# Kernel optimization log

Hardware: AMD Instinct MI355X
Metric: run time of the kernel (lower is better)

## Reference

```python
import jax, jax.numpy as jnp
import numpy as np

B, S, H = 4, 2048, 1024   # batch, seq_len, hidden_dim
E, D = 8, 1024            # num_experts, expert_dim (== hidden per module structure)
TOP_K = 2


def setup_inputs() -> dict:
    key = jax.random.key(0)
    ks = jax.random.split(key, 8)
    scale_h = 1.0 / np.sqrt(H)
    scale_d = 1.0 / np.sqrt(D)
    return {
        "x": jax.random.normal(ks[0], (B, S, H), dtype=jnp.float32),
        # router linear: hidden -> num_experts
        "w_router": jax.random.normal(ks[1], (H, E), dtype=jnp.float32) * scale_h,
        "b_router": jnp.zeros((E,), dtype=jnp.float32),
        # per-expert linear: hidden -> expert_dim
        "w_experts": jax.random.normal(ks[2], (E, H, D), dtype=jnp.float32) * scale_h,
        "b_experts": jnp.zeros((E, D), dtype=jnp.float32),
        # output linear: expert_dim -> expert_dim
        "w_out": jax.random.normal(ks[3], (D, D), dtype=jnp.float32) * scale_d,
        "b_out": jnp.zeros((D,), dtype=jnp.float32),
    }


def reference(x, w_router, b_router, w_experts, b_experts, w_out, b_out):
    # --- MoERouter: softmax over expert logits, top-2, renormalize ---
    logits = jnp.einsum("bsh,he->bse", x, w_router) + b_router          # [B,S,E]
    probs = jax.nn.softmax(logits, axis=-1)
    top_p, top_i = jax.lax.top_k(probs, TOP_K)                           # [B,S,2]
    top_p = top_p / jnp.sum(top_p, axis=-1, keepdims=True)
    # --- Dense expert compute over all tokens (module computes every expert) ---
    expert_out = jnp.einsum("bsh,ehd->bsed", x, w_experts) + b_experts   # [B,S,E,D]
    expert_out = jax.nn.gelu(expert_out)
    # --- Gather top-2 expert outputs and combine with routing weights ---
    sel = jnp.take_along_axis(expert_out, top_i[..., None], axis=2)      # [B,S,2,D]
    combined = jnp.sum(sel * top_p[..., None], axis=2)                   # [B,S,D]
    # --- Output projection ---
    return jnp.einsum("bsd,de->bse", combined, w_out) + b_out
```

## Files before the change

kernel.cpp:

```cpp
#include <hip/hip_runtime.h>


#define TOKENS 8192
#define HDIM   1024
#define DDIM   1024
#define NEXP   8

typedef __bf16 bf16x8 __attribute__((ext_vector_type(8)));
typedef float  f32x4  __attribute__((ext_vector_type(4)));

__device__ __forceinline__ unsigned short f2b(float f) {
  unsigned int u = __builtin_bit_cast(unsigned int, f);
  u = u + 0x7fffu + ((u >> 16) & 1u);
  return (unsigned short)(u >> 16);
}
__device__ __forceinline__ float b2f(unsigned short b) {
  unsigned int u = ((unsigned int)b) << 16;
  return __builtin_bit_cast(float, u);
}

__device__ __forceinline__ void gld_lds16(const void* g, void* l) {
  __builtin_amdgcn_global_load_lds(
      (__attribute__((address_space(1))) void*)(g),
      (__attribute__((address_space(3))) void*)(l),
      16, 0, 0);
}


__global__ void transpose_cvt_kernel(const float* __restrict__ we, const float* __restrict__ wo,
                                     unsigned short* __restrict__ weT, unsigned short* __restrict__ woT) {
  __shared__ unsigned short tile[32][33];
  int z = blockIdx.z;
  const float* s;
  unsigned short* d;
  if (z < 8) { s = we + (size_t)z * HDIM * DDIM; d = weT + (size_t)z * HDIM * DDIM; }
  else       { s = wo;                            d = woT; }
  int bx = blockIdx.x * 32;
  int by = blockIdx.y * 32;
  for (int i = threadIdx.y; i < 32; i += 8)
    tile[i][threadIdx.x] = f2b(s[(size_t)(by + i) * 1024 + bx + threadIdx.x]);
  __syncthreads();
  for (int i = threadIdx.y; i < 32; i += 8)
    d[(size_t)(bx + i) * 1024 + by + threadIdx.x] = tile[threadIdx.x][i];
}


__global__ void router_compute_kernel(const float* __restrict__ x, const float* __restrict__ wr,
                                      const float* __restrict__ br,
                                      int* __restrict__ eidx, float* __restrict__ ew,
                                      unsigned short* __restrict__ xb) {
  int wave = threadIdx.x >> 6, lane = threadIdx.x & 63;
  int t = blockIdx.x * 4 + wave;
  const float* xp = x + (size_t)t * HDIM;
  unsigned short* xbp = xb + (size_t)t * HDIM;
  float acc[8];
#pragma unroll
  for (int e = 0; e < 8; ++e) acc[e] = 0.f;
#pragma unroll
  for (int h0 = 0; h0 < HDIM; h0 += 256) {
    int h = h0 + lane * 4;
    float4 xv = *(const float4*)&xp[h];
    ushort4 o;
    o.x = f2b(xv.x); o.y = f2b(xv.y); o.z = f2b(xv.z); o.w = f2b(xv.w);
    *(ushort4*)&xbp[h] = o;
    float xq[4] = {xv.x, xv.y, xv.z, xv.w};
#pragma unroll
    for (int q = 0; q < 4; ++q) {
      const float4* wp = (const float4*)&wr[(h + q) * 8];
      float4 w0 = wp[0], w1 = wp[1];
      acc[0] += xq[q] * w0.x; acc[1] += xq[q] * w0.y; acc[2] += xq[q] * w0.z; acc[3] += xq[q] * w0.w;
      acc[4] += xq[q] * w1.x; acc[5] += xq[q] * w1.y; acc[6] += xq[q] * w1.z; acc[7] += xq[q] * w1.w;
    }
  }
#pragma unroll
  for (int off = 32; off; off >>= 1)
#pragma unroll
    for (int e = 0; e < 8; ++e) acc[e] += __shfl_xor(acc[e], off, 64);
  if (lane == 0) {
    float l[8], p[8];
    float m = -1e30f;
#pragma unroll
    for (int e = 0; e < 8; ++e) { l[e] = acc[e] + br[e]; m = fmaxf(m, l[e]); }
    float s = 0.f;
#pragma unroll
    for (int e = 0; e < 8; ++e) { p[e] = __expf(l[e] - m); s += p[e]; }
    int i1 = 0;
#pragma unroll
    for (int e = 1; e < 8; ++e) if (p[e] > p[i1]) i1 = e;
    int i2 = (i1 == 0) ? 1 : 0;
#pragma unroll
    for (int e = 0; e < 8; ++e) if (e != i1 && p[e] > p[i2]) i2 = e;
    float ps = p[i1] + p[i2];
    eidx[t * 2]     = i1;  ew[t * 2]     = p[i1] / ps;
    eidx[t * 2 + 1] = i2;  ew[t * 2 + 1] = p[i2] / ps;
  }
}


__global__ __launch_bounds__(1024) void build_lists_kernel(
    const int* __restrict__ eidx, const float* ew,
    int* __restrict__ counts, int* __restrict__ tok2, float* __restrict__ wl,
    int* s2p) {
  int e = blockIdx.x;
  int tid = threadIdx.x;
  int lane = tid & 63, wv = tid >> 6;
  __shared__ int wsum[16];
  __shared__ int base;
  if (tid == 0) base = 0;
  __syncthreads();
  for (int c = 0; c < 2 * TOKENS; c += 1024) {
    int i = c + tid;
    bool m = (eidx[i] == e);
    unsigned long long bal = __ballot(m);
    if (lane == 0) wsum[wv] = __popcll(bal);
    __syncthreads();
    int wbase = base;
    for (int w = 0; w < wv; ++w) wbase += wsum[w];
    if (m) {
      int pos = wbase + __popcll(bal & ((1ull << lane) - 1ull));
      float w = ew[i];
      tok2[e * TOKENS + pos] = i;
      wl[e * TOKENS + pos] = w;
      s2p[i] = pos;
    }
    int total = 0;
#pragma unroll
    for (int w = 0; w < 16; ++w) total += wsum[w];
    __syncthreads();
    if (tid == 0) base += total;
    __syncthreads();
  }
  if (tid == 0) counts[e] = base;
}


__global__ __launch_bounds__(256, 3) void expert_gemm_kernel(
    const unsigned short* __restrict__ xb, const unsigned short* __restrict__ weT,
    const float* __restrict__ b_experts, const int* __restrict__ counts,
    const int* __restrict__ tok2, const float* __restrict__ wlist,
    unsigned short* __restrict__ outE) {
  int b = blockIdx.x;
  int id = (b >> 3) + (b & 7) * 512;
  int e = id >> 9;
  int rem = id & 511;
  int m0 = (rem >> 3) << 7;
  int n0 = (rem & 7) << 7;
  int cnt = counts[e];
  if (m0 >= cnt) return;
  int cbase = 0;
  for (int q = 0; q < e; ++q) cbase += counts[q];

  __shared__ unsigned short As[3][128 * 32];
  __shared__ unsigned short Bs[3][128 * 32];
  __shared__ int   tokS[128];
  __shared__ float wS[128];

  int tid = threadIdx.x;
  if (tid < 128) {
    int r = m0 + tid;
    tokS[tid] = (r < cnt) ? tok2[e * TOKENS + r] : 0;
    wS[tid]   = (r < cnt) ? wlist[e * TOKENS + r] : 0.f;
  }
  __syncthreads();

  int wave = tid >> 6, lane = tid & 63;
  int subr = lane >> 2, koff = (lane & 3) * 8;

  const unsigned short* wbase = weT + (size_t)e * (HDIM * DDIM);
  const unsigned short* asrc[2];
  const unsigned short* bsrc[2];
  unsigned short* adst[3][2];
  unsigned short* bdst[3][2];
#pragma unroll
  for (int i = 0; i < 2; ++i) {
    int row = i * 64 + wave * 16 + subr;
    asrc[i] = xb + (size_t)(tokS[row] >> 1) * HDIM + koff;
    bsrc[i] = wbase + (size_t)(n0 + row) * HDIM + koff;
#pragma unroll
    for (int bb = 0; bb < 3; ++bb) {
      adst[bb][i] = &As[bb][i * 2048 + wave * 512];
      bdst[bb][i] = &Bs[bb][i * 2048 + wave * 512];
    }
  }

  int wm = wave & 1, wn = wave >> 1;
  int quad = lane >> 4, lr = lane & 15;

  f32x4 zero = {0.f, 0.f, 0.f, 0.f};
  f32x4 acc[4][4];
#pragma unroll
  for (int i = 0; i < 4; ++i)
#pragma unroll
    for (int j = 0; j < 4; ++j) acc[i][j] = zero;

#pragma unroll
  for (int s = 0; s < 2; ++s)
#pragma unroll
    for (int i = 0; i < 2; ++i) {
      gld_lds16(asrc[i] + s * 32, adst[s][i]);
      gld_lds16(bsrc[i] + s * 32, bdst[s][i]);
    }

#pragma unroll
  for (int kk = 0; kk < 32; ++kk) {
    if (kk < 31) asm volatile("s_waitcnt vmcnt(4)" ::: "memory");
    else         asm volatile("s_waitcnt vmcnt(0)" ::: "memory");
    __builtin_amdgcn_s_barrier();
    if (kk + 2 < 32) {
      int nb = (kk + 2) % 3;
      int off = (kk + 2) * 32;
#pragma unroll
      for (int i = 0; i < 2; ++i) {
        gld_lds16(asrc[i] + off, adst[nb][i]);
        gld_lds16(bsrc[i] + off, bdst[nb][i]);
      }
    }
    int cb = kk % 3;
    bf16x8 af[4], bfr[4];
#pragma unroll
    for (int i = 0; i < 4; ++i)
      af[i] = *(const bf16x8*)&As[cb][(wm * 64 + i * 16 + lr) * 32 + quad * 8];
#pragma unroll
    for (int j = 0; j < 4; ++j)
      bfr[j] = *(const bf16x8*)&Bs[cb][(wn * 64 + j * 16 + lr) * 32 + quad * 8];
#pragma unroll
    for (int i = 0; i < 4; ++i)
#pragma unroll
      for (int j = 0; j < 4; ++j)
        acc[i][j] = __builtin_amdgcn_mfma_f32_16x16x32_bf16(af[i], bfr[j], acc[i][j], 0, 0, 0);
  }

  int rowbase = cbase + m0;
#pragma unroll
  for (int j = 0; j < 4; ++j) {
    int col = n0 + wn * 64 + j * 16 + lr;
    float bias = b_experts[e * DDIM + col];
#pragma unroll
    for (int i = 0; i < 4; ++i) {
      int rbase = wm * 64 + i * 16 + quad * 4;
#pragma unroll
      for (int r = 0; r < 4; ++r) {
        int row = rbase + r;
        if (m0 + row < cnt) {
          float h = acc[i][j][r] + bias;
          float z = 0.7978845608f * (h + 0.044715f * h * h * h);
          float t = 1.f - 2.f / (__expf(2.f * z) + 1.f);
          float g = 0.5f * h * (1.f + t);
          outE[(size_t)(rowbase + row) * DDIM + col] = f2b(g * wS[row]);
        }
      }
    }
  }
}


__global__ void combine_kernel(const ushort4* __restrict__ outE,
                               const int* __restrict__ eidx, const int* __restrict__ s2p,
                               const int* __restrict__ counts,
                               ushort4* __restrict__ comb) {
  __shared__ int cbase[8];
  int tid = threadIdx.x;
  if (tid < 8) {
    int s = 0;
    for (int q = 0; q < tid; ++q) s += counts[q];
    cbase[tid] = s;
  }
  __syncthreads();
  int t = blockIdx.x;
  int d4 = tid;
  int i0 = t * 2, i1 = i0 + 1;
  size_t r0 = ((size_t)(cbase[eidx[i0]] + s2p[i0])) * 256 + d4;
  size_t r1 = ((size_t)(cbase[eidx[i1]] + s2p[i1])) * 256 + d4;
  ushort4 a = outE[r0];
  ushort4 b = outE[r1];
  ushort4 o;
  o.x = f2b(b2f(a.x) + b2f(b.x));
  o.y = f2b(b2f(a.y) + b2f(b.y));
  o.z = f2b(b2f(a.z) + b2f(b.z));
  o.w = f2b(b2f(a.w) + b2f(b.w));
  comb[t * 256 + d4] = o;
}


__global__ __launch_bounds__(256, 3) void out_gemm_kernel(
    const unsigned short* __restrict__ Abf, const unsigned short* __restrict__ BT,
    const float* __restrict__ bias, float* __restrict__ out) {
  int b = blockIdx.x;
  int id = (b >> 3) + (b & 7) * 64;
  int n0 = (id >> 6) << 7;
  int m0 = (id & 63) << 7;

  __shared__ unsigned short As[3][128 * 32];
  __shared__ unsigned short Bs[3][128 * 32];
  int tid = threadIdx.x, wave = tid >> 6, lane = tid & 63;
  int subr = lane >> 2, koff = (lane & 3) * 8;

  const unsigned short* asrc[2];
  const unsigned short* bsrc[2];
  unsigned short* adst[3][2];
  unsigned short* bdst[3][2];
#pragma unroll
  for (int i = 0; i < 2; ++i) {
    int row = i * 64 + wave * 16 + subr;
    asrc[i] = Abf + (size_t)(m0 + row) * DDIM + koff;
    bsrc[i] = BT + (size_t)(n0 + row) * DDIM + koff;
#pragma unroll
    for (int bb = 0; bb < 3; ++bb) {
      adst[bb][i] = &As[bb][i * 2048 + wave * 512];
      bdst[bb][i] = &Bs[bb][i * 2048 + wave * 512];
    }
  }

  int wm = wave & 1, wn = wave >> 1;
  int quad = lane >> 4, lr = lane & 15;

  f32x4 zero = {0.f, 0.f, 0.f, 0.f};
  f32x4 acc[4][4];
#pragma unroll
  for (int i = 0; i < 4; ++i)
#pragma unroll
    for (int j = 0; j < 4; ++j) acc[i][j] = zero;

#pragma unroll
  for (int s = 0; s < 2; ++s)
#pragma unroll
    for (int i = 0; i < 2; ++i) {
      gld_lds16(asrc[i] + s * 32, adst[s][i]);
      gld_lds16(bsrc[i] + s * 32, bdst[s][i]);
    }

#pragma unroll
  for (int kk = 0; kk < 32; ++kk) {
    if (kk < 31) asm volatile("s_waitcnt vmcnt(4)" ::: "memory");
    else         asm volatile("s_waitcnt vmcnt(0)" ::: "memory");
    __builtin_amdgcn_s_barrier();
    if (kk + 2 < 32) {
      int nb = (kk + 2) % 3;
      int off = (kk + 2) * 32;
#pragma unroll
      for (int i = 0; i < 2; ++i) {
        gld_lds16(asrc[i] + off, adst[nb][i]);
        gld_lds16(bsrc[i] + off, bdst[nb][i]);
      }
    }
    int cb = kk % 3;
    bf16x8 af[4], bfr[4];
#pragma unroll
    for (int i = 0; i < 4; ++i)
      af[i] = *(const bf16x8*)&As[cb][(wm * 64 + i * 16 + lr) * 32 + quad * 8];
#pragma unroll
    for (int j = 0; j < 4; ++j)
      bfr[j] = *(const bf16x8*)&Bs[cb][(wn * 64 + j * 16 + lr) * 32 + quad * 8];
#pragma unroll
    for (int i = 0; i < 4; ++i)
#pragma unroll
      for (int j = 0; j < 4; ++j)
        acc[i][j] = __builtin_amdgcn_mfma_f32_16x16x32_bf16(af[i], bfr[j], acc[i][j], 0, 0, 0);
  }

#pragma unroll
  for (int j = 0; j < 4; ++j) {
    int col = n0 + wn * 64 + j * 16 + lr;
    float bs = bias[col];
#pragma unroll
    for (int i = 0; i < 4; ++i) {
      int rbase = wm * 64 + i * 16 + quad * 4;
#pragma unroll
      for (int r = 0; r < 4; ++r)
        out[(size_t)(m0 + rbase + r) * DDIM + col] = acc[i][j][r] + bs;
    }
  }
}


extern "C" void kernel_launch(void* const* d_in, const int* in_sizes, int n_in,
                              void* d_out, int out_size, void* d_ws, size_t ws_size,
                              hipStream_t stream) {
  const float* x  = (const float*)d_in[0];
  const float* wr = (const float*)d_in[1];
  const float* br = (const float*)d_in[2];
  const float* we = (const float*)d_in[3];
  const float* be = (const float*)d_in[4];
  const float* wo = (const float*)d_in[5];
  const float* bo = (const float*)d_in[6];
  float* out = (float*)d_out;

  char* ws = (char*)d_ws;
  unsigned short* xb      = (unsigned short*)(ws);
  unsigned short* weT     = (unsigned short*)(ws + 16777216);
  unsigned short* woT     = (unsigned short*)(ws + 33554432);
  unsigned short* outE    = (unsigned short*)(ws + 35651584);
  int*            counts  = (int*)           (ws + 69206016);
  int*            tok2    = (int*)           (ws + 69206272);
  float*          wlist   = (float*)         (ws + 69468416);
  int*            eidx    = (int*)           (ws + 69730560);
  float*          ew      = (float*)         (ws + 69796096);
  int*            s2p     = (int*)ew;
  unsigned short* comb    = xb;

  router_compute_kernel<<<2048, 256, 0, stream>>>(x, wr, br, eidx, ew, xb);
  transpose_cvt_kernel<<<dim3(32, 32, 9), dim3(32, 8), 0, stream>>>(we, wo, weT, woT);
  build_lists_kernel<<<8, 1024, 0, stream>>>(eidx, ew, counts, tok2, wlist, s2p);
  expert_gemm_kernel<<<4096, 256, 0, stream>>>(xb, weT, be, counts, tok2, wlist, outE);
  combine_kernel<<<8192, 256, 0, stream>>>((const ushort4*)outE, eidx, s2p, counts, (ushort4*)comb);
  out_gemm_kernel<<<512, 256, 0, stream>>>(comb, woT, bo, out);
}
```

Before: 282.3 us.

## Restructure expert GEMM into 256x256 tiles with 8 waves and phased pipeline

The grouped expert GEMM moves from 128x128 tiles with 4 waves to 256x256 tiles with 8 waves. Each wave now computes 128x64 outputs through a 4-phase schedule per 64-wide K step, interleaving global-to-LDS loads with MFMA bursts that run under raised priority. The LDS layout is XOR-swizzled to cut bank conflicts, and the block-to-expert mapping now interleaves experts. The larger tiles raise data reuse and reduce global traffic, but they also mean more padded work wasted on each expert's partial last M tile and higher register pressure.

```diff
diff --git a/kernel.cpp b/kernel.cpp
--- a/kernel.cpp
+++ b/kernel.cpp
@@ -134,119 +134,135 @@
 }
 
 
-__global__ __launch_bounds__(256, 3) void expert_gemm_kernel(
+#define MFMA_ROW(MH, MI, AF) \
+  acc[(MH)*4+(MI)][0] = __builtin_amdgcn_mfma_f32_16x16x32_bf16(AF, bF0, acc[(MH)*4+(MI)][0], 0, 0, 0); \
+  acc[(MH)*4+(MI)][1] = __builtin_amdgcn_mfma_f32_16x16x32_bf16(AF, bF1, acc[(MH)*4+(MI)][1], 0, 0, 0); \
+  acc[(MH)*4+(MI)][2] = __builtin_amdgcn_mfma_f32_16x16x32_bf16(AF, bF2, acc[(MH)*4+(MI)][2], 0, 0, 0); \
+  acc[(MH)*4+(MI)][3] = __builtin_amdgcn_mfma_f32_16x16x32_bf16(AF, bF3, acc[(MH)*4+(MI)][3], 0, 0, 0);
+
+#define PHASE(KS, MH, STAGE_CODE, TRAIL_CODE) do { \
+  const int abase_ = (cur * 2 + (KS)) * 8192; \
+  const bf16x8 aF0 = *(const bf16x8*)&As[abase_ + (arow0 + (MH)*64 +  0) * 32 + cs8]; \
+  const bf16x8 aF1 = *(const bf16x8*)&As[abase_ + (arow0 + (MH)*64 + 16) * 32 + cs8]; \
+  const bf16x8 aF2 = *(const bf16x8*)&As[abase_ + (arow0 + (MH)*64 + 32) * 32 + cs8]; \
+  const bf16x8 aF3 = *(const bf16x8*)&As[abase_ + (arow0 + (MH)*64 + 48) * 32 + cs8]; \
+  const bf16x8 bF0 = *(const bf16x8*)&Bs[abase_ + (brow0 +  0) * 32 + cs8]; \
+  const bf16x8 bF1 = *(const bf16x8*)&Bs[abase_ + (brow0 + 16) * 32 + cs8]; \
+  const bf16x8 bF2 = *(const bf16x8*)&Bs[abase_ + (brow0 + 32) * 32 + cs8]; \
+  const bf16x8 bF3 = *(const bf16x8*)&Bs[abase_ + (brow0 + 48) * 32 + cs8]; \
+  STAGE_CODE; \
+  asm volatile("" ::: "memory"); \
+  __builtin_amdgcn_s_barrier(); \
+  __builtin_amdgcn_s_setprio(1); \
+  MFMA_ROW(MH, 0, aF0) \
+  MFMA_ROW(MH, 1, aF1) \
+  MFMA_ROW(MH, 2, aF2) \
+  MFMA_ROW(MH, 3, aF3) \
+  __builtin_amdgcn_s_setprio(0); \
+  TRAIL_CODE; \
+  asm volatile("" ::: "memory"); \
+  __builtin_amdgcn_s_barrier(); \
+} while (0)
+
+__global__ __launch_bounds__(512, 2) void expert_gemm_kernel(
     const unsigned short* __restrict__ xb, const unsigned short* __restrict__ weT,
     const float* __restrict__ b_experts, const int* __restrict__ counts,
     const int* __restrict__ tok2, const float* __restrict__ wlist,
     unsigned short* __restrict__ outE) {
   int b = blockIdx.x;
-  int id = (b >> 3) + (b & 7) * 512;
-  int e = id >> 9;
-  int rem = id & 511;
-  int m0 = (rem >> 3) << 7;
-  int n0 = (rem & 7) << 7;
+  int e = b & 7;
+  int tt = b >> 3;
+  int m0 = (tt >> 2) << 8;
+  int n0 = (tt & 3) << 8;
   int cnt = counts[e];
   if (m0 >= cnt) return;
   int cbase = 0;
   for (int q = 0; q < e; ++q) cbase += counts[q];
 
-  __shared__ unsigned short As[3][128 * 32];
-  __shared__ unsigned short Bs[3][128 * 32];
-  __shared__ int   tokS[128];
-  __shared__ float wS[128];
+  __shared__ unsigned short As[2 * 2 * 8192];
+  __shared__ unsigned short Bs[2 * 2 * 8192];
+  __shared__ int   tokS[256];
+  __shared__ float wS[256];
 
   int tid = threadIdx.x;
-  if (tid < 128) {
+  if (tid < 256) {
     int r = m0 + tid;
     tokS[tid] = (r < cnt) ? tok2[e * TOKENS + r] : 0;
     wS[tid]   = (r < cnt) ? wlist[e * TOKENS + r] : 0.f;
   }
   __syncthreads();
 
-  int wave = tid >> 6, lane = tid & 63;
-  int subr = lane >> 2, koff = (lane & 3) * 8;
-
   const unsigned short* wbase = weT + (size_t)e * (HDIM * DDIM);
-  const unsigned short* asrc[2];
-  const unsigned short* bsrc[2];
-  unsigned short* adst[3][2];
-  unsigned short* bdst[3][2];
-#pragma unroll
-  for (int i = 0; i < 2; ++i) {
-    int row = i * 64 + wave * 16 + subr;
-    asrc[i] = xb + (size_t)(tokS[row] >> 1) * HDIM + koff;
-    bsrc[i] = wbase + (size_t)(n0 + row) * HDIM + koff;
-#pragma unroll
-    for (int bb = 0; bb < 3; ++bb) {
-      adst[bb][i] = &As[bb][i * 2048 + wave * 512];
-      bdst[bb][i] = &Bs[bb][i * 2048 + wave * 512];
-    }
-  }
-
-  int wm = wave & 1, wn = wave >> 1;
-  int quad = lane >> 4, lr = lane & 15;
-
-  f32x4 zero = {0.f, 0.f, 0.f, 0.f};
-  f32x4 acc[4][4];
-#pragma unroll
-  for (int i = 0; i < 4; ++i)
-#pragma unroll
-    for (int j = 0; j < 4; ++j) acc[i][j] = zero;
-
-#pragma unroll
-  for (int s = 0; s < 2; ++s)
-#pragma unroll
-    for (int i = 0; i < 2; ++i) {
-      gld_lds16(asrc[i] + s * 32, adst[s][i]);
-      gld_lds16(bsrc[i] + s * 32, bdst[s][i]);
-    }
-
-#pragma unroll
-  for (int kk = 0; kk < 32; ++kk) {
-    if (kk < 31) asm volatile("s_waitcnt vmcnt(4)" ::: "memory");
-    else         asm volatile("s_waitcnt vmcnt(0)" ::: "memory");
-    __builtin_amdgcn_s_barrier();
-    if (kk + 2 < 32) {
-      int nb = (kk + 2) % 3;
-      int off = (kk + 2) * 32;
-#pragma unroll
-      for (int i = 0; i < 2; ++i) {
-        gld_lds16(asrc[i] + off, adst[nb][i]);
-        gld_lds16(bsrc[i] + off, bdst[nb][i]);
-      }
-    }
-    int cb = kk % 3;
-    bf16x8 af[4], bfr[4];
-#pragma unroll
-    for (int i = 0; i < 4; ++i)
-      af[i] = *(const bf16x8*)&As[cb][(wm * 64 + i * 16 + lr) * 32 + quad * 8];
-#pragma unroll
-    for (int j = 0; j < 4; ++j)
-      bfr[j] = *(const bf16x8*)&Bs[cb][(wn * 64 + j * 16 + lr) * 32 + quad * 8];
-#pragma unroll
-    for (int i = 0; i < 4; ++i)
-#pragma unroll
-      for (int j = 0; j < 4; ++j)
-        acc[i][j] = __builtin_amdgcn_mfma_f32_16x16x32_bf16(af[i], bfr[j], acc[i][j], 0, 0, 0);
+  int g0 = tid, g1 = 512 + tid;
+  int r0 = g0 >> 2, r1 = g1 >> 2;
+  int sc0 = (((g0 & 3) ^ (r0 & 3)) << 3);
+  int sc1 = (((g1 & 3) ^ (r1 & 3)) << 3);
+  const unsigned short* aS0 = xb + (size_t)(tokS[r0] >> 1) * HDIM + sc0;
+  const unsigned short* aS1 = xb + (size_t)(tokS[r1] >> 1) * HDIM + sc1;
+  const unsigned short* bS0 = wbase + (size_t)(n0 + r0) * HDIM + sc0;
+  const unsigned short* bS1 = wbase + (size_t)(n0 + r1) * HDIM + sc1;
+  int du0 = (tid & ~63) * 8;
+  int du1 = (512 + (tid & ~63)) * 8;
+
+  int wid = tid >> 6, lane = tid & 63;
+  int wm = wid >> 2, wn = wid & 3;
+  int lr = lane & 15, quad = lane >> 4;
+  int cs8 = ((quad ^ (lane & 3)) << 3);
+  int arow0 = wm * 128 + lr;
+  int brow0 = wn * 64 + lr;
+
+  f32x4 acc[8][4];
+#pragma unroll
+  for (int i = 0; i < 8; ++i)
+#pragma unroll
+    for (int j = 0; j < 4; ++j) acc[i][j] = (f32x4){0.f, 0.f, 0.f, 0.f};
+
+  gld_lds16(aS0 +  0, &As[0 * 8192 + du0]); gld_lds16(aS1 +  0, &As[0 * 8192 + du1]);
+  gld_lds16(bS0 +  0, &Bs[0 * 8192 + du0]); gld_lds16(bS1 +  0, &Bs[0 * 8192 + du1]);
+  gld_lds16(aS0 + 32, &As[1 * 8192 + du0]); gld_lds16(aS1 + 32, &As[1 * 8192 + du1]);
+  gld_lds16(bS0 + 32, &Bs[1 * 8192 + du0]); gld_lds16(bS1 + 32, &Bs[1 * 8192 + du1]);
+  gld_lds16(aS0 + 64, &As[2 * 8192 + du0]); gld_lds16(aS1 + 64, &As[2 * 8192 + du1]);
+  gld_lds16(bS0 + 64, &Bs[2 * 8192 + du0]); gld_lds16(bS1 + 64, &Bs[2 * 8192 + du1]);
+  __syncthreads();
+
+  for (int t = 0; t < 16; ++t) {
+    int cur = t & 1;
+    PHASE(0, 0,
+      { if (t < 15) { int kc = (t + 1) * 64 + 32; int db = ((cur ^ 1) * 2 + 1) * 8192;
+          gld_lds16(aS0 + kc, &As[db + du0]); gld_lds16(aS1 + kc, &As[db + du1]); } },
+      { });
+    PHASE(0, 1,
+      { if (t < 15) { int kc = (t + 1) * 64 + 32; int db = ((cur ^ 1) * 2 + 1) * 8192;
+          gld_lds16(bS0 + kc, &Bs[db + du0]); gld_lds16(bS1 + kc, &Bs[db + du1]); } },
+      { if (t < 15) asm volatile("s_waitcnt vmcnt(4)" ::: "memory");
+        else        asm volatile("s_waitcnt vmcnt(0)" ::: "memory"); });
+    PHASE(1, 0,
+      { if (t < 14) { int kc = (t + 2) * 64; int db = (cur * 2) * 8192;
+          gld_lds16(aS0 + kc, &As[db + du0]); gld_lds16(aS1 + kc, &As[db + du1]); } },
+      { });
+    PHASE(1, 1,
+      { if (t < 14) { int kc = (t + 2) * 64; int db = (cur * 2) * 8192;
+          gld_lds16(bS0 + kc, &Bs[db + du0]); gld_lds16(bS1 + kc, &Bs[db + du1]); } },
+      { asm volatile("s_waitcnt vmcnt(8)" ::: "memory"); });
   }
 
   int rowbase = cbase + m0;
 #pragma unroll
-  for (int j = 0; j < 4; ++j) {
-    int col = n0 + wn * 64 + j * 16 + lr;
+  for (int ni = 0; ni < 4; ++ni) {
+    int col = n0 + wn * 64 + ni * 16 + lr;
     float bias = b_experts[e * DDIM + col];
 #pragma unroll
-    for (int i = 0; i < 4; ++i) {
-      int rbase = wm * 64 + i * 16 + quad * 4;
+    for (int am = 0; am < 8; ++am) {
+      int rb = wm * 128 + am * 16 + quad * 4;
 #pragma unroll
       for (int r = 0; r < 4; ++r) {
-        int row = rbase + r;
+        int row = rb + r;
         if (m0 + row < cnt) {
-          float h = acc[i][j][r] + bias;
+          float h = acc[am][ni][r] + bias;
           float z = 0.7978845608f * (h + 0.044715f * h * h * h);
-          float t = 1.f - 2.f / (__expf(2.f * z) + 1.f);
-          float g = 0.5f * h * (1.f + t);
-          outE[(size_t)(rowbase + row) * DDIM + col] = f2b(g * wS[row]);
+          float tz = 1.f - 2.f / (__expf(2.f * z) + 1.f);
+          float gg = 0.5f * h * (1.f + tz);
+          outE[(size_t)(rowbase + row) * DDIM + col] = f2b(gg * wS[row]);
         }
       }
     }
@@ -401,7 +417,7 @@
   router_compute_kernel<<<2048, 256, 0, stream>>>(x, wr, br, eidx, ew, xb);
   transpose_cvt_kernel<<<dim3(32, 32, 9), dim3(32, 8), 0, stream>>>(we, wo, weT, woT);
   build_lists_kernel<<<8, 1024, 0, stream>>>(eidx, ew, counts, tok2, wlist, s2p);
-  expert_gemm_kernel<<<4096, 256, 0, stream>>>(xb, weT, be, counts, tok2, wlist, outE);
+  expert_gemm_kernel<<<1024, 512, 0, stream>>>(xb, weT, be, counts, tok2, wlist, outE);
   combine_kernel<<<8192, 256, 0, stream>>>((const ushort4*)outE, eidx, s2p, counts, (ushort4*)comb);
   out_gemm_kernel<<<512, 256, 0, stream>>>(comb, woT, bo, out);
 }
```

New measurement: 330.2 us. 1.17x slower.

## Fuse router, weight transpose and list building into one pre-kernel using atomics

Applied to the files above, without the earlier changes.

Merges the router, the weight transpose/convert and the expert list construction into a single launch, with block ranges split by role. The serial 8-block list-building kernel is replaced by per-token atomicAdd slot allocation on the expert counters, which are zeroed by a memset. This removes two launches and a low-parallelism scan pass. The cost is that token order inside each expert list becomes nondeterministic, and atomics contend on eight counters.

```diff
diff --git a/kernel.cpp b/kernel.cpp
--- a/kernel.cpp
+++ b/kernel.cpp
@@ -27,29 +27,35 @@
 }
 
 
-__global__ void transpose_cvt_kernel(const float* __restrict__ we, const float* __restrict__ wo,
-                                     unsigned short* __restrict__ weT, unsigned short* __restrict__ woT) {
+__global__ __launch_bounds__(256) void pre_kernel(
+    const float* __restrict__ x, const float* __restrict__ wr,
+    const float* __restrict__ br,
+    const float* __restrict__ we, const float* __restrict__ wo,
+    unsigned short* __restrict__ weT, unsigned short* __restrict__ woT,
+    unsigned short* __restrict__ xb,
+    int* __restrict__ eidx, int* __restrict__ counts,
+    int* __restrict__ tok2, float* __restrict__ wlist, int* __restrict__ s2p) {
   __shared__ unsigned short tile[32][33];
-  int z = blockIdx.z;
-  const float* s;
-  unsigned short* d;
-  if (z < 8) { s = we + (size_t)z * HDIM * DDIM; d = weT + (size_t)z * HDIM * DDIM; }
-  else       { s = wo;                            d = woT; }
-  int bx = blockIdx.x * 32;
-  int by = blockIdx.y * 32;
-  for (int i = threadIdx.y; i < 32; i += 8)
-    tile[i][threadIdx.x] = f2b(s[(size_t)(by + i) * 1024 + bx + threadIdx.x]);
-  __syncthreads();
-  for (int i = threadIdx.y; i < 32; i += 8)
-    d[(size_t)(bx + i) * 1024 + by + threadIdx.x] = tile[threadIdx.x][i];
-}
-
-
-__global__ void router_compute_kernel(const float* __restrict__ x, const float* __restrict__ wr,
-                                      const float* __restrict__ br,
-                                      int* __restrict__ eidx, float* __restrict__ ew,
-                                      unsigned short* __restrict__ xb) {
-  int wave = threadIdx.x >> 6, lane = threadIdx.x & 63;
+  int tid = threadIdx.x;
+  if (blockIdx.x >= 2048) {
+    int lid = blockIdx.x - 2048;
+    int z = lid >> 10;
+    int rem = lid & 1023;
+    int bx = (rem & 31) * 32;
+    int by = (rem >> 5) * 32;
+    const float* s;
+    unsigned short* d;
+    if (z < 8) { s = we + (size_t)z * HDIM * DDIM; d = weT + (size_t)z * HDIM * DDIM; }
+    else       { s = wo;                            d = woT; }
+    int tx = tid & 31, ty = tid >> 5;
+    for (int i = ty; i < 32; i += 8)
+      tile[i][tx] = f2b(s[(size_t)(by + i) * 1024 + bx + tx]);
+    __syncthreads();
+    for (int i = ty; i < 32; i += 8)
+      d[(size_t)(bx + i) * 1024 + by + tx] = tile[tx][i];
+    return;
+  }
+  int wave = tid >> 6, lane = tid & 63;
   int t = blockIdx.x * 4 + wave;
   const float* xp = x + (size_t)t * HDIM;
   unsigned short* xbp = xb + (size_t)t * HDIM;
@@ -91,46 +97,13 @@
 #pragma unroll
     for (int e = 0; e < 8; ++e) if (e != i1 && p[e] > p[i2]) i2 = e;
     float ps = p[i1] + p[i2];
-    eidx[t * 2]     = i1;  ew[t * 2]     = p[i1] / ps;
-    eidx[t * 2 + 1] = i2;  ew[t * 2 + 1] = p[i2] / ps;
-  }
-}
-
-
-__global__ __launch_bounds__(1024) void build_lists_kernel(
-    const int* __restrict__ eidx, const float* ew,
-    int* __restrict__ counts, int* __restrict__ tok2, float* __restrict__ wl,
-    int* s2p) {
-  int e = blockIdx.x;
-  int tid = threadIdx.x;
-  int lane = tid & 63, wv = tid >> 6;
-  __shared__ int wsum[16];
-  __shared__ int base;
-  if (tid == 0) base = 0;
-  __syncthreads();
-  for (int c = 0; c < 2 * TOKENS; c += 1024) {
-    int i = c + tid;
-    bool m = (eidx[i] == e);
-    unsigned long long bal = __ballot(m);
-    if (lane == 0) wsum[wv] = __popcll(bal);
-    __syncthreads();
-    int wbase = base;
-    for (int w = 0; w < wv; ++w) wbase += wsum[w];
-    if (m) {
-      int pos = wbase + __popcll(bal & ((1ull << lane) - 1ull));
-      float w = ew[i];
-      tok2[e * TOKENS + pos] = i;
-      wl[e * TOKENS + pos] = w;
-      s2p[i] = pos;
-    }
-    int total = 0;
-#pragma unroll
-    for (int w = 0; w < 16; ++w) total += wsum[w];
-    __syncthreads();
-    if (tid == 0) base += total;
-    __syncthreads();
-  }
-  if (tid == 0) counts[e] = base;
+    int p1 = atomicAdd(&counts[i1], 1);
+    int p2 = atomicAdd(&counts[i2], 1);
+    eidx[t * 2]     = i1;
+    eidx[t * 2 + 1] = i2;
+    tok2[i1 * TOKENS + p1] = t * 2;      wlist[i1 * TOKENS + p1] = p[i1] / ps;  s2p[t * 2]     = p1;
+    tok2[i2 * TOKENS + p2] = t * 2 + 1;  wlist[i2 * TOKENS + p2] = p[i2] / ps;  s2p[t * 2 + 1] = p2;
+  }
 }
 
 
@@ -394,13 +367,12 @@
   int*            tok2    = (int*)           (ws + 69206272);
   float*          wlist   = (float*)         (ws + 69468416);
   int*            eidx    = (int*)           (ws + 69730560);
-  float*          ew      = (float*)         (ws + 69796096);
-  int*            s2p     = (int*)ew;
+  int*            s2p     = (int*)           (ws + 69796096);
   unsigned short* comb    = xb;
 
-  router_compute_kernel<<<2048, 256, 0, stream>>>(x, wr, br, eidx, ew, xb);
-  transpose_cvt_kernel<<<dim3(32, 32, 9), dim3(32, 8), 0, stream>>>(we, wo, weT, woT);
-  build_lists_kernel<<<8, 1024, 0, stream>>>(eidx, ew, counts, tok2, wlist, s2p);
+  hipMemsetAsync(counts, 0, NEXP * sizeof(int), stream);
+  pre_kernel<<<2048 + 9216, 256, 0, stream>>>(x, wr, br, we, wo, weT, woT,
+                                              xb, eidx, counts, tok2, wlist, s2p);
   expert_gemm_kernel<<<4096, 256, 0, stream>>>(xb, weT, be, counts, tok2, wlist, outE);
   combine_kernel<<<8192, 256, 0, stream>>>((const ushort4*)outE, eidx, s2p, counts, (ushort4*)comb);
   out_gemm_kernel<<<512, 256, 0, stream>>>(comb, woT, bo, out);
```

Result: slower. 420.3 us (+48.9%).

## Fuse top-2 combine into output GEMM A-load and merge router with weight transpose

Applied to the files above, without the earlier changes.

The separate combine kernel is removed. The output GEMM now gathers the two expert rows per token through registers, sums them in bf16 and writes the result to LDS as its A tile, using a double buffer instead of the triple-buffered async LDS loads. The router and the weight transpose/convert kernels are merged into one launch with a block-index split. This saves the combine write/read round trip and one launch, at the cost of register-path A loads, a shallower pipeline and an extra full barrier per k-step in the GEMM.

```diff
diff --git a/kernel.cpp b/kernel.cpp
--- a/kernel.cpp
+++ b/kernel.cpp
@@ -8,6 +8,7 @@
 
 typedef __bf16 bf16x8 __attribute__((ext_vector_type(8)));
 typedef float  f32x4  __attribute__((ext_vector_type(4)));
+typedef unsigned short u16x8 __attribute__((ext_vector_type(8)));
 
 __device__ __forceinline__ unsigned short f2b(float f) {
   unsigned int u = __builtin_bit_cast(unsigned int, f);
@@ -27,29 +28,34 @@
 }
 
 
-__global__ void transpose_cvt_kernel(const float* __restrict__ we, const float* __restrict__ wo,
-                                     unsigned short* __restrict__ weT, unsigned short* __restrict__ woT) {
+__global__ __launch_bounds__(256) void pre_kernel(
+    const float* __restrict__ x, const float* __restrict__ wr,
+    const float* __restrict__ br,
+    const float* __restrict__ we, const float* __restrict__ wo,
+    unsigned short* __restrict__ weT, unsigned short* __restrict__ woT,
+    unsigned short* __restrict__ xb,
+    int* __restrict__ eidx, float* __restrict__ ew) {
   __shared__ unsigned short tile[32][33];
-  int z = blockIdx.z;
-  const float* s;
-  unsigned short* d;
-  if (z < 8) { s = we + (size_t)z * HDIM * DDIM; d = weT + (size_t)z * HDIM * DDIM; }
-  else       { s = wo;                            d = woT; }
-  int bx = blockIdx.x * 32;
-  int by = blockIdx.y * 32;
-  for (int i = threadIdx.y; i < 32; i += 8)
-    tile[i][threadIdx.x] = f2b(s[(size_t)(by + i) * 1024 + bx + threadIdx.x]);
-  __syncthreads();
-  for (int i = threadIdx.y; i < 32; i += 8)
-    d[(size_t)(bx + i) * 1024 + by + threadIdx.x] = tile[threadIdx.x][i];
-}
-
-
-__global__ void router_compute_kernel(const float* __restrict__ x, const float* __restrict__ wr,
-                                      const float* __restrict__ br,
-                                      int* __restrict__ eidx, float* __restrict__ ew,
-                                      unsigned short* __restrict__ xb) {
-  int wave = threadIdx.x >> 6, lane = threadIdx.x & 63;
+  int tid = threadIdx.x;
+  if (blockIdx.x >= 2048) {
+    int lid = blockIdx.x - 2048;
+    int z = lid >> 10;
+    int rem = lid & 1023;
+    int bx = (rem & 31) * 32;
+    int by = (rem >> 5) * 32;
+    const float* s;
+    unsigned short* d;
+    if (z < 8) { s = we + (size_t)z * HDIM * DDIM; d = weT + (size_t)z * HDIM * DDIM; }
+    else       { s = wo;                            d = woT; }
+    int tx = tid & 31, ty = tid >> 5;
+    for (int i = ty; i < 32; i += 8)
+      tile[i][tx] = f2b(s[(size_t)(by + i) * 1024 + bx + tx]);
+    __syncthreads();
+    for (int i = ty; i < 32; i += 8)
+      d[(size_t)(bx + i) * 1024 + by + tx] = tile[tx][i];
+    return;
+  }
+  int wave = tid >> 6, lane = tid & 63;
   int t = blockIdx.x * 4 + wave;
   const float* xp = x + (size_t)t * HDIM;
   unsigned short* xbp = xb + (size_t)t * HDIM;
@@ -254,62 +260,50 @@
 }
 
 
-__global__ void combine_kernel(const ushort4* __restrict__ outE,
-                               const int* __restrict__ eidx, const int* __restrict__ s2p,
-                               const int* __restrict__ counts,
-                               ushort4* __restrict__ comb) {
-  __shared__ int cbase[8];
-  int tid = threadIdx.x;
-  if (tid < 8) {
-    int s = 0;
-    for (int q = 0; q < tid; ++q) s += counts[q];
-    cbase[tid] = s;
-  }
-  __syncthreads();
-  int t = blockIdx.x;
-  int d4 = tid;
-  int i0 = t * 2, i1 = i0 + 1;
-  size_t r0 = ((size_t)(cbase[eidx[i0]] + s2p[i0])) * 256 + d4;
-  size_t r1 = ((size_t)(cbase[eidx[i1]] + s2p[i1])) * 256 + d4;
-  ushort4 a = outE[r0];
-  ushort4 b = outE[r1];
-  ushort4 o;
-  o.x = f2b(b2f(a.x) + b2f(b.x));
-  o.y = f2b(b2f(a.y) + b2f(b.y));
-  o.z = f2b(b2f(a.z) + b2f(b.z));
-  o.w = f2b(b2f(a.w) + b2f(b.w));
-  comb[t * 256 + d4] = o;
-}
-
-
-__global__ __launch_bounds__(256, 3) void out_gemm_kernel(
-    const unsigned short* __restrict__ Abf, const unsigned short* __restrict__ BT,
+__global__ __launch_bounds__(256) void out_gemm_kernel(
+    const unsigned short* __restrict__ outE, const unsigned short* __restrict__ BT,
+    const int* __restrict__ eidx, const int* __restrict__ s2p,
+    const int* __restrict__ counts,
     const float* __restrict__ bias, float* __restrict__ out) {
   int b = blockIdx.x;
   int id = (b >> 3) + (b & 7) * 64;
   int n0 = (id >> 6) << 7;
   int m0 = (id & 63) << 7;
 
-  __shared__ unsigned short As[3][128 * 32];
-  __shared__ unsigned short Bs[3][128 * 32];
+  __shared__ unsigned short As[2][128 * 32];
+  __shared__ unsigned short Bs[2][128 * 32];
+  __shared__ int cbase[8];
+
   int tid = threadIdx.x, wave = tid >> 6, lane = tid & 63;
   int subr = lane >> 2, koff = (lane & 3) * 8;
 
-  const unsigned short* asrc[2];
+  if (tid < 8) {
+    int s = 0;
+    for (int q = 0; q < tid; ++q) s += counts[q];
+    cbase[tid] = s;
+  }
+  __syncthreads();
+
+  const unsigned short* pA[2];
+  const unsigned short* pB_[2];
   const unsigned short* bsrc[2];
-  unsigned short* adst[3][2];
-  unsigned short* bdst[3][2];
+  unsigned short* bdst[2][2];
 #pragma unroll
   for (int i = 0; i < 2; ++i) {
     int row = i * 64 + wave * 16 + subr;
-    asrc[i] = Abf + (size_t)(m0 + row) * DDIM + koff;
+    int t = m0 + row;
+    int i0 = 2 * t, i1 = 2 * t + 1;
+    pA[i]  = outE + (size_t)(cbase[eidx[i0]] + s2p[i0]) * DDIM + koff;
+    pB_[i] = outE + (size_t)(cbase[eidx[i1]] + s2p[i1]) * DDIM + koff;
     bsrc[i] = BT + (size_t)(n0 + row) * DDIM + koff;
 #pragma unroll
-    for (int bb = 0; bb < 3; ++bb) {
-      adst[bb][i] = &As[bb][i * 2048 + wave * 512];
+    for (int bb = 0; bb < 2; ++bb)
       bdst[bb][i] = &Bs[bb][i * 2048 + wave * 512];
-    }
-  }
+  }
+  int adst_off[2];
+#pragma unroll
+  for (int i = 0; i < 2; ++i)
+    adst_off[i] = i * 2048 + wave * 512 + lane * 8;
 
   int wm = wave & 1, wn = wave >> 1;
   int quad = lane >> 4, lr = lane & 15;
@@ -321,41 +315,55 @@
 #pragma unroll
     for (int j = 0; j < 4; ++j) acc[i][j] = zero;
 
-#pragma unroll
-  for (int s = 0; s < 2; ++s)
-#pragma unroll
-    for (int i = 0; i < 2; ++i) {
-      gld_lds16(asrc[i] + s * 32, adst[s][i]);
-      gld_lds16(bsrc[i] + s * 32, bdst[s][i]);
-    }
-
-#pragma unroll
+  u16x8 ra[2], rb[2];
+#pragma unroll
+  for (int i = 0; i < 2; ++i) {
+    ra[i] = *(const u16x8*)(pA[i]);
+    rb[i] = *(const u16x8*)(pB_[i]);
+    gld_lds16(bsrc[i], bdst[0][i]);
+  }
+#pragma unroll
+  for (int i = 0; i < 2; ++i) {
+    u16x8 o;
+#pragma unroll
+    for (int q = 0; q < 8; ++q) o[q] = f2b(b2f(ra[i][q]) + b2f(rb[i][q]));
+    *(u16x8*)&As[0][adst_off[i]] = o;
+  }
+  __syncthreads();
+
   for (int kk = 0; kk < 32; ++kk) {
-    if (kk < 31) asm volatile("s_waitcnt vmcnt(4)" ::: "memory");
-    else         asm volatile("s_waitcnt vmcnt(0)" ::: "memory");
-    __builtin_amdgcn_s_barrier();
-    if (kk + 2 < 32) {
-      int nb = (kk + 2) % 3;
-      int off = (kk + 2) * 32;
+    int cur = kk & 1, nxt = cur ^ 1;
+    if (kk < 31) {
+      int off = (kk + 1) * 32;
 #pragma unroll
       for (int i = 0; i < 2; ++i) {
-        gld_lds16(asrc[i] + off, adst[nb][i]);
-        gld_lds16(bsrc[i] + off, bdst[nb][i]);
+        ra[i] = *(const u16x8*)(pA[i] + off);
+        rb[i] = *(const u16x8*)(pB_[i] + off);
+        gld_lds16(bsrc[i] + off, bdst[nxt][i]);
       }
     }
-    int cb = kk % 3;
     bf16x8 af[4], bfr[4];
 #pragma unroll
     for (int i = 0; i < 4; ++i)
-      af[i] = *(const bf16x8*)&As[cb][(wm * 64 + i * 16 + lr) * 32 + quad * 8];
+      af[i] = *(const bf16x8*)&As[cur][(wm * 64 + i * 16 + lr) * 32 + quad * 8];
 #pragma unroll
     for (int j = 0; j < 4; ++j)
-      bfr[j] = *(const bf16x8*)&Bs[cb][(wn * 64 + j * 16 + lr) * 32 + quad * 8];
+      bfr[j] = *(const bf16x8*)&Bs[cur][(wn * 64 + j * 16 + lr) * 32 + quad * 8];
 #pragma unroll
     for (int i = 0; i < 4; ++i)
 #pragma unroll
       for (int j = 0; j < 4; ++j)
         acc[i][j] = __builtin_amdgcn_mfma_f32_16x16x32_bf16(af[i], bfr[j], acc[i][j], 0, 0, 0);
+    if (kk < 31) {
+#pragma unroll
+      for (int i = 0; i < 2; ++i) {
+        u16x8 o;
+#pragma unroll
+        for (int q = 0; q < 8; ++q) o[q] = f2b(b2f(ra[i][q]) + b2f(rb[i][q]));
+        *(u16x8*)&As[nxt][adst_off[i]] = o;
+      }
+    }
+    __syncthreads();
   }
 
 #pragma unroll
@@ -396,12 +404,10 @@
   int*            eidx    = (int*)           (ws + 69730560);
   float*          ew      = (float*)         (ws + 69796096);
   int*            s2p     = (int*)ew;
-  unsigned short* comb    = xb;
-
-  router_compute_kernel<<<2048, 256, 0, stream>>>(x, wr, br, eidx, ew, xb);
-  transpose_cvt_kernel<<<dim3(32, 32, 9), dim3(32, 8), 0, stream>>>(we, wo, weT, woT);
+
+  pre_kernel<<<2048 + 9216, 256, 0, stream>>>(x, wr, br, we, wo, weT, woT,
+                                              xb, eidx, ew);
   build_lists_kernel<<<8, 1024, 0, stream>>>(eidx, ew, counts, tok2, wlist, s2p);
   expert_gemm_kernel<<<4096, 256, 0, stream>>>(xb, weT, be, counts, tok2, wlist, outE);
-  combine_kernel<<<8192, 256, 0, stream>>>((const ushort4*)outE, eidx, s2p, counts, (ushort4*)comb);
-  out_gemm_kernel<<<512, 256, 0, stream>>>(comb, woT, bo, out);
-}
+  out_gemm_kernel<<<512, 256, 0, stream>>>(outE, woT, eidx, s2p, counts, bo, out);
+}
```

Result: slower. 293.7 us (+4.0%).
